# Optimization experiments

Hardware: AMD Instinct MI355X
Metric: run time of the kernel (lower is better)

## Reference

```python
import jax, jax.numpy as jnp
import numpy as np

B, N = 16, 4096
D_IN, D_OUT, HID, E = 128, 128, 256, 8
SG_HID = 16  # SharedGate hidden fixed at 16 in __init__


def setup_inputs() -> dict:
    key = jax.random.key(0)
    ks = jax.random.split(key, 6)
    s = 0.05
    return {
        "x": jax.random.normal(ks[0], (B, N, D_IN), dtype=jnp.float32),
        "active_experts": jnp.ones((B, E), dtype=jnp.int32),
        # SharedGate: fc1 [16, D_IN], fc2 [D_IN, 16] (torch Linear weight is [out, in])
        "sg_w1": jax.random.normal(ks[1], (SG_HID, D_IN), dtype=jnp.float32) * s,
        "sg_w2": jax.random.normal(ks[2], (D_IN, SG_HID), dtype=jnp.float32) * s,
        # TaskSpecificGate: E linears [1, D_IN] -> stacked [E, D_IN]
        "gate_w": jax.random.normal(ks[3], (E, D_IN), dtype=jnp.float32) * s,
        # Expert MLPs (no bias): fc1 [E, HID, D_IN], fc2 [E, D_OUT, HID]
        "exp_w1": jax.random.normal(ks[4], (E, HID, D_IN), dtype=jnp.float32) * s,
        "exp_w2": jax.random.normal(ks[5], (E, D_OUT, HID), dtype=jnp.float32) * s,
    }


def reference(x, active_experts, sg_w1, sg_w2, gate_w, exp_w1, exp_w2):
    b, n, d_in = x.shape
    xf = x.reshape(-1, d_in)  # [T, D_IN], T = B*N (node-level routing)

    # SharedGate with residual: fc2(relu(fc1(x))) + x
    shared = jnp.maximum(xf @ sg_w1.T, 0.0) @ sg_w2.T + xf  # [T, D_IN]

    # Task-specific gate: per-expert scalar scores, masked softmax over experts
    scores = (shared @ gate_w.T).reshape(b, n, -1)  # [B, N, E]
    mask = active_experts.astype(bool)[:, None, :]  # [B, 1, E]
    masked = jnp.where(mask, scores, -jnp.inf)
    weights = jax.nn.softmax(masked, axis=-1)  # [B, N, E]

    # All experts (dense): batched two-layer MLP per expert
    h = jnp.maximum(jnp.einsum("td,ehd->teh", xf, exp_w1), 0.0)  # [T, E, HID]
    out = jnp.einsum("teh,eoh->teo", h, exp_w2)  # [T, E, D_OUT]
    out_r = out.reshape(b, n, weights.shape[-1], -1)  # [B, N, E, D_OUT]

    # Gate-weighted combine over experts
    output_end = jnp.sum(out_r * weights[..., None], axis=2)  # [B, N, D_OUT]
    aux_loss = jnp.float32(0.0)  # sign=False
    return output_end, aux_loss
```

## Files before the change

kernel.cpp:

```cpp
#include <hip/hip_runtime.h>
#include <hip/hip_bf16.h>


typedef float f32x4 __attribute__((ext_vector_type(4)));
typedef short bf16x8 __attribute__((ext_vector_type(8)));

static __device__ __forceinline__ short f2bs(float f) {
  union { __hip_bfloat16 b; short s; } u;
  u.b = __float2bfloat16(f);
  return u.s;
}

static __device__ __forceinline__ unsigned pk2(float lo, float hi) {
  union { __hip_bfloat162 b; unsigned u; } t;
  t.b = __float22bfloat162_rn(make_float2(lo, hi));
  return t.u;
}


__global__ void prep_kernel(const float* __restrict__ sg_w1,
                            const float* __restrict__ sg_w2,
                            const float* __restrict__ gate_w,
                            const float* __restrict__ exp_w1,
                            const float* __restrict__ exp_w2,
                            short* __restrict__ ws_s) {
  int idx = blockIdx.x * 256 + threadIdx.x;
  if (idx < 262144) {
    int e = idx >> 15, rem = idx & 32767;
    int frag = rem >> 9, lane = (rem >> 3) & 63, j = rem & 7;
    int hid = (frag >> 2) * 16 + (lane & 15);
    int k   = (frag & 3) * 32 + (lane >> 4) * 8 + j;
    ws_s[idx] = f2bs(exp_w1[(e * 256 + hid) * 128 + k]);
  } else if (idx < 524288) {
    int i2 = idx - 262144;
    int e = i2 >> 15, rem = i2 & 32767;
    int frag = rem >> 9, lane = (rem >> 3) & 63, j = rem & 7;
    int lg = lane >> 4, l15 = lane & 15;
    int ks = frag >> 3;
    int oi = frag & 7;
    int o  = oi * 16 + l15;
    int h  = ks * 32 + (j < 4 ? lg * 4 + j : 16 + lg * 4 + (j - 4));
    ws_s[idx] = f2bs(exp_w2[(e * 128 + o) * 256 + h]);
  } else if (idx < 526336) {
    int i3 = idx - 524288;
    int k = i3 >> 9, lane = (i3 >> 3) & 63, j = i3 & 7;
    int lg = lane >> 4, l15 = lane & 15;
    ws_s[idx] = f2bs(sg_w1[l15 * 128 + k * 32 + lg * 8 + j]);
  } else if (idx < 528384) {
    int i4 = idx - 526336;
    int k = i4 >> 9, lane = (i4 >> 3) & 63, j = i4 & 7;
    int lg = lane >> 4, l15 = lane & 15;
    ws_s[idx] = (l15 < 8) ? f2bs(gate_w[l15 * 128 + k * 32 + lg * 8 + j]) : (short)0;
  } else if (idx < 528896) {
    int i5 = idx - 528384;
    int lane = (i5 >> 3) & 63, j = i5 & 7;
    int lg = lane >> 4, l15 = lane & 15;
    int kk = lg * 8 + j;
    if (l15 < 8 && kk < 16) {
      float acc = 0.f;
      for (int d = 0; d < 128; ++d) acc += gate_w[l15 * 128 + d] * sg_w2[d * 16 + kk];
      ws_s[idx] = f2bs(acc);
    } else {
      ws_s[idx] = 0;
    }
  }
}

__global__ __launch_bounds__(256, 2) void moe_kernel(
    const float* __restrict__ x, const int* __restrict__ active,
    const short* __restrict__ ws_s, float* __restrict__ out) {
  __shared__ __align__(16) short Wring[4][8192];
  __shared__ short Ul[4][1280];

  const short* W1p  = ws_s;
  const short* W2p  = ws_s + 262144;
  const short* sg1p = ws_s + 524288;
  const short* gwp  = ws_s + 526336;
  const short* gcp  = ws_s + 528384;

  const int tid  = threadIdx.x;
  const int lane = tid & 63;
  const int wid  = tid >> 6;
  const int l15  = lane & 15;
  const int lg   = lane >> 4;
  const int tokw = blockIdx.x * 128 + wid * 32;

  auto stage = [&](int c) {
    int buf = c & 3;
#pragma unroll
    for (int t = 0; t < 4; ++t) {
      int f = wid * 4 + t;
      const short* s = (f < 8)
          ? (W1p + ((size_t)c * 8 + f) * 512 + lane * 8)
          : (W2p + ((size_t)c * 8 + (f - 8)) * 512 + lane * 8);
      __builtin_amdgcn_global_load_lds(
          (const __attribute__((address_space(1))) void*)s,
          (__attribute__((address_space(3))) void*)(&Wring[buf][f * 512]),
          16, 0, 0);
    }
  };
  auto waitv = [&](int n) {
    if (n == 8)      asm volatile("s_waitcnt vmcnt(8)" ::: "memory");
    else if (n == 4) asm volatile("s_waitcnt vmcnt(4)" ::: "memory");
    else             asm volatile("s_waitcnt vmcnt(0)" ::: "memory");
    __builtin_amdgcn_sched_barrier(0);
  };

  stage(0);
  stage(1);

  short* Ulw = &Ul[wid][0];
  for (int i = lane; i < 640; i += 64) ((int*)Ulw)[i] = 0;

  bf16x8 xf[2][4];
  {
    int trow = tokw + l15;
#pragma unroll
    for (int m = 0; m < 2; ++m) {
      const float* xr = x + (size_t)(trow + m * 16) * 128;
#pragma unroll
      for (int k = 0; k < 4; ++k) {
        int c = k * 32 + lg * 8;
        float4 a = *(const float4*)(xr + c);
        float4 b = *(const float4*)(xr + c + 4);
        bf16x8 v;
        v[0] = f2bs(a.x); v[1] = f2bs(a.y); v[2] = f2bs(a.z); v[3] = f2bs(a.w);
        v[4] = f2bs(b.x); v[5] = f2bs(b.y); v[6] = f2bs(b.z); v[7] = f2bs(b.w);
        xf[m][k] = v;
      }
    }
  }
  __syncthreads();

  f32x4 wreg[2];
  {
    bf16x8 sgf[4], gwf[4];
#pragma unroll
    for (int k = 0; k < 4; ++k) {
      sgf[k] = *(const bf16x8*)(sg1p + k * 512 + lane * 8);
      gwf[k] = *(const bf16x8*)(gwp  + k * 512 + lane * 8);
    }
#pragma unroll
    for (int m = 0; m < 2; ++m) {
      f32x4 acc = {0.f, 0.f, 0.f, 0.f};
#pragma unroll
      for (int k = 0; k < 4; ++k)
        acc = __builtin_amdgcn_mfma_f32_16x16x32_bf16(xf[m][k], sgf[k], acc, 0, 0, 0);
#pragma unroll
      for (int r = 0; r < 4; ++r)
        Ulw[(m * 16 + lg * 4 + r) * 40 + l15] = f2bs(fmaxf(acc[r], 0.f));
    }
    f32x4 sc[2];
#pragma unroll
    for (int m = 0; m < 2; ++m) {
      f32x4 acc = {0.f, 0.f, 0.f, 0.f};
#pragma unroll
      for (int k = 0; k < 4; ++k)
        acc = __builtin_amdgcn_mfma_f32_16x16x32_bf16(xf[m][k], gwf[k], acc, 0, 0, 0);
      sc[m] = acc;
    }
    __syncthreads();
    bf16x8 gcf = *(const bf16x8*)(gcp + lane * 8);
#pragma unroll
    for (int m = 0; m < 2; ++m) {
      bf16x8 uf = *(const bf16x8*)(Ulw + (m * 16 + l15) * 40 + lg * 8);
      sc[m] = __builtin_amdgcn_mfma_f32_16x16x32_bf16(uf, gcf, sc[m], 0, 0, 0);
    }
    int b = tokw >> 12;
    float am = (l15 < 8 && active[b * 8 + l15] != 0) ? 0.f : -3.0e38f;
#pragma unroll
    for (int m = 0; m < 2; ++m) {
      f32x4 w4;
#pragma unroll
      for (int r = 0; r < 4; ++r) {
        float s = sc[m][r] + am;
        float mx = s;
        mx = fmaxf(mx, __shfl_xor(mx, 1));
        mx = fmaxf(mx, __shfl_xor(mx, 2));
        mx = fmaxf(mx, __shfl_xor(mx, 4));
        float p = __expf(s - mx);
        float su = p;
        su += __shfl_xor(su, 1);
        su += __shfl_xor(su, 2);
        su += __shfl_xor(su, 4);
        w4[r] = p / su;
      }
      wreg[m] = w4;
    }
  }

  f32x4 acc2[2][8];
#pragma unroll
  for (int m = 0; m < 2; ++m)
#pragma unroll
    for (int o = 0; o < 8; ++o)
      acc2[m][o] = {0.f, 0.f, 0.f, 0.f};

  for (int e = 0; e < 8; ++e) {
    float wv[2];
    {
      int srcb = ((l15 >> 2) << 4) | e;
      int rp = l15 & 3;
#pragma unroll
      for (int m = 0; m < 2; ++m) {
        float q0 = __shfl(wreg[m][0], srcb), q1 = __shfl(wreg[m][1], srcb);
        float q2 = __shfl(wreg[m][2], srcb), q3 = __shfl(wreg[m][3], srcb);
        float lo = (rp & 1) ? q1 : q0, hi = (rp & 1) ? q3 : q2;
        wv[m] = (rp & 2) ? hi : lo;
      }
    }

#pragma unroll
    for (int ks = 0; ks < 8; ++ks) {
      const int c = e * 8 + ks;
      if (c + 2 < 64) stage(c + 2);
      waitv(c <= 61 ? 8 : (c == 62 ? 4 : 0));
      __builtin_amdgcn_s_barrier();

      const short* wb = &Wring[c & 3][0];
      bf16x8 Af[8], Bf[8];
#pragma unroll
      for (int i = 0; i < 8; ++i) {
        Af[i] = *(const bf16x8*)(wb + i * 512 + lane * 8);
        Bf[i] = *(const bf16x8*)(wb + 4096 + i * 512 + lane * 8);
      }

      f32x4 a1[2][2];
#pragma unroll
      for (int m = 0; m < 2; ++m)
#pragma unroll
        for (int n = 0; n < 2; ++n) {
          f32x4 acc = {0.f, 0.f, 0.f, 0.f};
#pragma unroll
          for (int kx = 0; kx < 4; ++kx)
            acc = __builtin_amdgcn_mfma_f32_16x16x32_bf16(Af[n * 4 + kx], xf[m][kx], acc, 0, 0, 0);
          a1[m][n] = acc;
        }
      bf16x8 hB[2];
#pragma unroll
      for (int m = 0; m < 2; ++m) {
        float s = wv[m];
        union { unsigned u[4]; bf16x8 v; } hb;
        hb.u[0] = pk2(fmaxf(a1[m][0][0], 0.f) * s, fmaxf(a1[m][0][1], 0.f) * s);
        hb.u[1] = pk2(fmaxf(a1[m][0][2], 0.f) * s, fmaxf(a1[m][0][3], 0.f) * s);
        hb.u[2] = pk2(fmaxf(a1[m][1][0], 0.f) * s, fmaxf(a1[m][1][1], 0.f) * s);
        hb.u[3] = pk2(fmaxf(a1[m][1][2], 0.f) * s, fmaxf(a1[m][1][3], 0.f) * s);
        hB[m] = hb.v;
      }
#pragma unroll
      for (int o = 0; o < 8; ++o)
#pragma unroll
        for (int m = 0; m < 2; ++m)
          acc2[m][o] = __builtin_amdgcn_mfma_f32_16x16x32_bf16(Bf[o], hB[m], acc2[m][o], 0, 0, 0);
    }
  }

#pragma unroll
  for (int m = 0; m < 2; ++m)
#pragma unroll
    for (int o = 0; o < 8; ++o)
      *(f32x4*)(out + (size_t)(tokw + m * 16 + l15) * 128 + o * 16 + lg * 4) = acc2[m][o];

  if (blockIdx.x == 0 && tid == 0) out[8388608] = 0.0f;
}

extern "C" void kernel_launch(void* const* d_in, const int* in_sizes, int n_in,
                              void* d_out, int out_size, void* d_ws, size_t ws_size,
                              hipStream_t stream) {
  const float* x      = (const float*)d_in[0];
  const int*   act    = (const int*)d_in[1];
  const float* sg_w1  = (const float*)d_in[2];
  const float* sg_w2  = (const float*)d_in[3];
  const float* gate_w = (const float*)d_in[4];
  const float* exp_w1 = (const float*)d_in[5];
  const float* exp_w2 = (const float*)d_in[6];
  short* ws_s = (short*)d_ws;
  float* out = (float*)d_out;

  prep_kernel<<<2066, 256, 0, stream>>>(sg_w1, sg_w2, gate_w, exp_w1, exp_w2, ws_s);
  moe_kernel<<<512, 256, 0, stream>>>(x, act, ws_s, out);
}
```

Baseline: 82.47 us.

## Double tokens per wave to reuse staged expert weights across 64 tokens

Each wave now handles 64 tokens instead of 32 and each block 256 tokens, so every staged chunk of expert weights in LDS feeds twice as many MFMAs. The grid halves to 256 blocks and launch bounds drop to one block per SM to make room for the larger accumulator array. The inner chunk loop is no longer unrolled, fragments are loaded just in time, and s_setprio is raised around the MFMA section. This cuts per-token weight traffic and LDS reads, but lowers occupancy and leaves fewer blocks than CUs to hide latency.

```diff
diff --git a/kernel.cpp b/kernel.cpp
--- a/kernel.cpp
+++ b/kernel.cpp
@@ -66,11 +66,11 @@
   }
 }
 
-__global__ __launch_bounds__(256, 2) void moe_kernel(
+__global__ __launch_bounds__(256, 1) void moe_kernel(
     const float* __restrict__ x, const int* __restrict__ active,
     const short* __restrict__ ws_s, float* __restrict__ out) {
   __shared__ __align__(16) short Wring[4][8192];
-  __shared__ short Ul[4][1280];
+  __shared__ short Ul[4][2560];
 
   const short* W1p  = ws_s;
   const short* W2p  = ws_s + 262144;
@@ -83,7 +83,7 @@
   const int wid  = tid >> 6;
   const int l15  = lane & 15;
   const int lg   = lane >> 4;
-  const int tokw = blockIdx.x * 128 + wid * 32;
+  const int tokw = blockIdx.x * 256 + wid * 64;
 
   auto stage = [&](int c) {
     int buf = c & 3;
@@ -110,13 +110,13 @@
   stage(1);
 
   short* Ulw = &Ul[wid][0];
-  for (int i = lane; i < 640; i += 64) ((int*)Ulw)[i] = 0;
-
-  bf16x8 xf[2][4];
+  for (int i = lane; i < 1280; i += 64) ((int*)Ulw)[i] = 0;
+
+  bf16x8 xf[4][4];
   {
     int trow = tokw + l15;
 #pragma unroll
-    for (int m = 0; m < 2; ++m) {
+    for (int m = 0; m < 4; ++m) {
       const float* xr = x + (size_t)(trow + m * 16) * 128;
 #pragma unroll
       for (int k = 0; k < 4; ++k) {
@@ -132,7 +132,7 @@
   }
   __syncthreads();
 
-  f32x4 wreg[2];
+  f32x4 wreg[4];
   {
     bf16x8 sgf[4], gwf[4];
 #pragma unroll
@@ -141,7 +141,7 @@
       gwf[k] = *(const bf16x8*)(gwp  + k * 512 + lane * 8);
     }
 #pragma unroll
-    for (int m = 0; m < 2; ++m) {
+    for (int m = 0; m < 4; ++m) {
       f32x4 acc = {0.f, 0.f, 0.f, 0.f};
 #pragma unroll
       for (int k = 0; k < 4; ++k)
@@ -150,9 +150,9 @@
       for (int r = 0; r < 4; ++r)
         Ulw[(m * 16 + lg * 4 + r) * 40 + l15] = f2bs(fmaxf(acc[r], 0.f));
     }
-    f32x4 sc[2];
-#pragma unroll
-    for (int m = 0; m < 2; ++m) {
+    f32x4 sc[4];
+#pragma unroll
+    for (int m = 0; m < 4; ++m) {
       f32x4 acc = {0.f, 0.f, 0.f, 0.f};
 #pragma unroll
       for (int k = 0; k < 4; ++k)
@@ -162,14 +162,14 @@
     __syncthreads();
     bf16x8 gcf = *(const bf16x8*)(gcp + lane * 8);
 #pragma unroll
-    for (int m = 0; m < 2; ++m) {
+    for (int m = 0; m < 4; ++m) {
       bf16x8 uf = *(const bf16x8*)(Ulw + (m * 16 + l15) * 40 + lg * 8);
       sc[m] = __builtin_amdgcn_mfma_f32_16x16x32_bf16(uf, gcf, sc[m], 0, 0, 0);
     }
     int b = tokw >> 12;
     float am = (l15 < 8 && active[b * 8 + l15] != 0) ? 0.f : -3.0e38f;
 #pragma unroll
-    for (int m = 0; m < 2; ++m) {
+    for (int m = 0; m < 4; ++m) {
       f32x4 w4;
 #pragma unroll
       for (int r = 0; r < 4; ++r) {
@@ -189,20 +189,20 @@
     }
   }
 
-  f32x4 acc2[2][8];
-#pragma unroll
-  for (int m = 0; m < 2; ++m)
+  f32x4 acc2[4][8];
+#pragma unroll
+  for (int m = 0; m < 4; ++m)
 #pragma unroll
     for (int o = 0; o < 8; ++o)
       acc2[m][o] = {0.f, 0.f, 0.f, 0.f};
 
   for (int e = 0; e < 8; ++e) {
-    float wv[2];
+    float wv[4];
     {
       int srcb = ((l15 >> 2) << 4) | e;
       int rp = l15 & 3;
 #pragma unroll
-      for (int m = 0; m < 2; ++m) {
+      for (int m = 0; m < 4; ++m) {
         float q0 = __shfl(wreg[m][0], srcb), q1 = __shfl(wreg[m][1], srcb);
         float q2 = __shfl(wreg[m][2], srcb), q3 = __shfl(wreg[m][3], srcb);
         float lo = (rp & 1) ? q1 : q0, hi = (rp & 1) ? q3 : q2;
@@ -210,53 +210,48 @@
       }
     }
 
-#pragma unroll
+#pragma unroll 1
     for (int ks = 0; ks < 8; ++ks) {
       const int c = e * 8 + ks;
       if (c + 2 < 64) stage(c + 2);
       waitv(c <= 61 ? 8 : (c == 62 ? 4 : 0));
       __builtin_amdgcn_s_barrier();
 
-      const short* wb = &Wring[c & 3][0];
-      bf16x8 Af[8], Bf[8];
-#pragma unroll
-      for (int i = 0; i < 8; ++i) {
-        Af[i] = *(const bf16x8*)(wb + i * 512 + lane * 8);
-        Bf[i] = *(const bf16x8*)(wb + 4096 + i * 512 + lane * 8);
-      }
-
-      f32x4 a1[2][2];
-#pragma unroll
-      for (int m = 0; m < 2; ++m)
-#pragma unroll
-        for (int n = 0; n < 2; ++n) {
-          f32x4 acc = {0.f, 0.f, 0.f, 0.f};
+      const short* rb = &Wring[c & 3][0];
+      __builtin_amdgcn_s_setprio(1);
+
+      union HU { unsigned u[4]; bf16x8 v; };
+      HU hu[4];
+#pragma unroll
+      for (int n = 0; n < 2; ++n) {
+        bf16x8 Af[4];
+#pragma unroll
+        for (int kx = 0; kx < 4; ++kx)
+          Af[kx] = *(const bf16x8*)(rb + (n * 4 + kx) * 512 + lane * 8);
+#pragma unroll
+        for (int m = 0; m < 4; ++m) {
+          f32x4 a = {0.f, 0.f, 0.f, 0.f};
 #pragma unroll
           for (int kx = 0; kx < 4; ++kx)
-            acc = __builtin_amdgcn_mfma_f32_16x16x32_bf16(Af[n * 4 + kx], xf[m][kx], acc, 0, 0, 0);
-          a1[m][n] = acc;
+            a = __builtin_amdgcn_mfma_f32_16x16x32_bf16(Af[kx], xf[m][kx], a, 0, 0, 0);
+          float s = wv[m];
+          hu[m].u[n * 2]     = pk2(fmaxf(a[0], 0.f) * s, fmaxf(a[1], 0.f) * s);
+          hu[m].u[n * 2 + 1] = pk2(fmaxf(a[2], 0.f) * s, fmaxf(a[3], 0.f) * s);
         }
-      bf16x8 hB[2];
-#pragma unroll
-      for (int m = 0; m < 2; ++m) {
-        float s = wv[m];
-        union { unsigned u[4]; bf16x8 v; } hb;
-        hb.u[0] = pk2(fmaxf(a1[m][0][0], 0.f) * s, fmaxf(a1[m][0][1], 0.f) * s);
-        hb.u[1] = pk2(fmaxf(a1[m][0][2], 0.f) * s, fmaxf(a1[m][0][3], 0.f) * s);
-        hb.u[2] = pk2(fmaxf(a1[m][1][0], 0.f) * s, fmaxf(a1[m][1][1], 0.f) * s);
-        hb.u[3] = pk2(fmaxf(a1[m][1][2], 0.f) * s, fmaxf(a1[m][1][3], 0.f) * s);
-        hB[m] = hb.v;
-      }
-#pragma unroll
-      for (int o = 0; o < 8; ++o)
-#pragma unroll
-        for (int m = 0; m < 2; ++m)
-          acc2[m][o] = __builtin_amdgcn_mfma_f32_16x16x32_bf16(Bf[o], hB[m], acc2[m][o], 0, 0, 0);
-    }
-  }
-
-#pragma unroll
-  for (int m = 0; m < 2; ++m)
+      }
+#pragma unroll
+      for (int o = 0; o < 8; ++o) {
+        bf16x8 Bf = *(const bf16x8*)(rb + 4096 + o * 512 + lane * 8);
+#pragma unroll
+        for (int m = 0; m < 4; ++m)
+          acc2[m][o] = __builtin_amdgcn_mfma_f32_16x16x32_bf16(Bf, hu[m].v, acc2[m][o], 0, 0, 0);
+      }
+      __builtin_amdgcn_s_setprio(0);
+    }
+  }
+
+#pragma unroll
+  for (int m = 0; m < 4; ++m)
 #pragma unroll
     for (int o = 0; o < 8; ++o)
       *(f32x4*)(out + (size_t)(tokw + m * 16 + l15) * 128 + o * 16 + lg * 4) = acc2[m][o];
@@ -278,5 +273,5 @@
   float* out = (float*)d_out;
 
   prep_kernel<<<2066, 256, 0, stream>>>(sg_w1, sg_w2, gate_w, exp_w1, exp_w2, ws_s);
-  moe_kernel<<<512, 256, 0, stream>>>(x, act, ws_s, out);
-}
+  moe_kernel<<<256, 256, 0, stream>>>(x, act, ws_s, out);
+}
```

New measurement: 101.5 us. +23.1%, slower.
